# Kernel optimization log

Measured on AMD Instinct MI355X. Metric: run time of the kernel, lower is better.

Reference implementation:

```python
import jax, jax.numpy as jnp
import numpy as np

D_MODEL = 384
D_STATE = 64
D_CONV = 3
EXPAND = 2
HEADDIM = 64
NGROUPS = 1
CHUNK = 256
D_INNER = EXPAND * D_MODEL            # 768
NHEADS = D_INNER // HEADDIM           # 12
CONV_DIM = D_INNER + 2 * NGROUPS * D_STATE   # 896
D_IN_PROJ = 2 * D_INNER + 2 * NGROUPS * D_STATE + NHEADS  # 1676
EPS = 1e-5


def setup_inputs() -> dict:
    key = jax.random.key(0)
    ks = jax.random.split(key, 8)
    B, H, W = 16, 32, 32
    u = jax.random.normal(ks[0], (B, D_MODEL, H, W), jnp.float32)
    in_proj_w = jax.random.normal(ks[1], (D_IN_PROJ, D_MODEL), jnp.float32) / np.sqrt(D_MODEL)
    conv_w = jax.random.normal(ks[2], (CONV_DIM, 1, D_CONV, D_CONV), jnp.float32) / np.sqrt(D_CONV * D_CONV)
    conv_b = jax.random.normal(ks[3], (CONV_DIM,), jnp.float32) * 0.01
    # dt_bias init as in Mamba2.__init__
    dt = jnp.exp(jax.random.uniform(ks[4], (NHEADS,)) * (np.log(0.1) - np.log(0.001)) + np.log(0.001))
    dt = jnp.clip(dt, 1e-4, None)
    dt_bias = dt + jnp.log(-jnp.expm1(-dt))
    A_log = jnp.log(jax.random.uniform(ks[5], (NHEADS,), minval=1.0, maxval=16.0))
    D = jnp.ones((NHEADS,), jnp.float32)
    norm_w = jnp.ones((D_INNER,), jnp.float32)
    norm_b = jnp.zeros((D_INNER,), jnp.float32)
    out_proj_w = jax.random.normal(ks[6], (D_MODEL, D_INNER), jnp.float32) / np.sqrt(D_INNER)
    return {"u": u, "in_proj_w": in_proj_w, "conv_w": conv_w, "conv_b": conv_b,
            "dt_bias": dt_bias, "A_log": A_log, "D": D, "norm_w": norm_w,
            "norm_b": norm_b, "out_proj_w": out_proj_w}


def _chunk_scan(x, dt, A, Bm, Cm):
    """SSD chunked scan. x:(b,l,h,p) dt:(b,l,h) A:(h,) Bm,Cm:(b,l,g,n) -> (b,l,h,p)"""
    b, l, h, p = x.shape
    nc = l // CHUNK
    xc = x.reshape(b, nc, CHUNK, h, p)
    dtc = dt.reshape(b, nc, CHUNK, h)
    hpg = h // NGROUPS
    Bh = jnp.repeat(Bm.reshape(b, nc, CHUNK, NGROUPS, D_STATE), hpg, axis=3)  # (b,c,cs,h,n)
    Ch = jnp.repeat(Cm.reshape(b, nc, CHUNK, NGROUPS, D_STATE), hpg, axis=3)
    dA = dtc * A                                  # (b,c,cs,h)
    dA_cs = jnp.cumsum(dA, axis=2)                # cumulative log-decay within chunk
    # ---- intra-chunk (masked, attention-like) ----
    Lmat = jnp.exp(dA_cs[:, :, :, None, :] - dA_cs[:, :, None, :, :])  # (b,c,i,j,h)
    causal = jnp.tril(jnp.ones((CHUNK, CHUNK), bool))
    att = jnp.einsum('bcihn,bcjhn->bcijh', Ch, Bh) * Lmat * dtc[:, :, None, :, :]
    att = jnp.where(causal[None, None, :, :, None], att, 0.0)
    y_intra = jnp.einsum('bcijh,bcjhp->bcihp', att, xc)
    # ---- per-chunk end states ----
    decay_to_end = jnp.exp(dA_cs[:, :, -1:, :] - dA_cs)                 # (b,c,cs,h)
    states = jnp.einsum('bcjhn,bcjh,bcjhp->bchpn', Bh, decay_to_end * dtc, xc)
    chunk_decay = jnp.exp(dA_cs[:, :, -1, :])                           # (b,c,h)
    # ---- inter-chunk recurrence over the (few) chunks ----
    def step(carry, inp):
        st, dec = inp
        new = carry * dec[:, :, None, None] + st
        return new, carry  # emit state *before* this chunk
    init = jnp.zeros((b, h, p, D_STATE), x.dtype)
    _, prevs = jax.lax.scan(step, init, (jnp.moveaxis(states, 1, 0), jnp.moveaxis(chunk_decay, 1, 0)))
    prev_states = jnp.moveaxis(prevs, 0, 1)                             # (b,c,h,p,n)
    y_inter = jnp.einsum('bcihn,bcih,bchpn->bcihp', Ch, jnp.exp(dA_cs), prev_states)
    return (y_intra + y_inter).reshape(b, l, h, p)


def reference(u, in_proj_w, conv_w, conv_b, dt_bias, A_log, D, norm_w, norm_b, out_proj_w):
    B, C, H, W = u.shape
    L = H * W
    useq = u.reshape(B, C, L).transpose(0, 2, 1)                        # (B,L,C)
    zxbcdt = useq @ in_proj_w.T                                         # (B,L,D_IN_PROJ)
    z = zxbcdt[..., :D_INNER]
    xBC = zxbcdt[..., D_INNER:D_INNER + CONV_DIM]
    dt = jax.nn.softplus(zxbcdt[..., D_INNER + CONV_DIM:] + dt_bias)    # (B,L,NHEADS)
    # depthwise 3x3 conv over (H,W)
    xBC = xBC.reshape(B, H, W, CONV_DIM)
    kern = jnp.transpose(conv_w, (2, 3, 1, 0))                          # HWIO, groups=CONV_DIM
    xBC = jax.lax.conv_general_dilated(xBC, kern, (1, 1), 'SAME',
                                       dimension_numbers=('NHWC', 'HWIO', 'NHWC'),
                                       feature_group_count=CONV_DIM) + conv_b
    xBC = jax.nn.silu(xBC).reshape(B, L, CONV_DIM)
    x = xBC[..., :D_INNER].reshape(B, L, NHEADS, HEADDIM)
    Bm = xBC[..., D_INNER:D_INNER + NGROUPS * D_STATE].reshape(B, L, NGROUPS, D_STATE)
    Cm = xBC[..., D_INNER + NGROUPS * D_STATE:].reshape(B, L, NGROUPS, D_STATE)
    A = -jnp.exp(A_log)
    y = _chunk_scan(x, dt, A, Bm, Cm) + D[None, None, :, None] * x      # D skip per head
    y = y.reshape(B, L, D_INNER)
    # LayerNorm then gate by z (no activation on z, matching source)
    mu = jnp.mean(y, axis=-1, keepdims=True)
    var = jnp.var(y, axis=-1, keepdims=True)
    y = (y - mu) / jnp.sqrt(var + EPS) * norm_w + norm_b
    y = y * z
    out = y @ out_proj_w.T                                              # (B,L,C)
    return out.reshape(B, H, W, C).transpose(0, 3, 1, 2)
```

## Files before the change

kernel.cpp:

```cpp
#include <hip/hip_runtime.h>
#include <hip/hip_bf16.h>

#define B_    16
#define L_    1024
#define DM    384
#define DIP   1676
#define NIP   1664
#define DI    768
#define CONVD 896
#define NH    12
#define HD    64
#define DS    64
#define NCH   4
#define CH    256
#define EPS_  1e-5f

typedef unsigned short u16;
typedef unsigned int   u32;
typedef __attribute__((ext_vector_type(8))) _Float16 f16x8;
typedef __attribute__((ext_vector_type(4))) float f32x4;

union U4 { uint4 v; u16 s[8]; };

#define SWZ(row, slot) (((row) << 7) + ((((slot) ^ ((row) & 7)) & 7) << 4))

__device__ __forceinline__ u16 f2h(float v) { return __builtin_bit_cast(u16, (_Float16)v); }
__device__ __forceinline__ float h2f(u16 h) { return (float)__builtin_bit_cast(_Float16, h); }

__global__ __launch_bounds__(256) void k_prep(
    const float* __restrict__ u, const float* __restrict__ ipw,
    const float* __restrict__ opw,
    const float* __restrict__ dtb, const float* __restrict__ A_log,
    u16* __restrict__ Ah, u16* __restrict__ Whip, u16* __restrict__ Woh,
    float* __restrict__ dt, float* __restrict__ dAcs, float* __restrict__ cdecay)
{
  __shared__ float smem[32 * 129 + 8];
  const int bid = blockIdx.x;
  const int t = threadIdx.x;
  if (bid < 1536) {
    float (*Ls)[129] = (float(*)[129])smem;
    const int l0 = (bid & 7) * 128;
    const int k0 = ((bid >> 3) % 12) * 32;
    const int b  = bid / 96;
#pragma unroll
    for (int r = 0; r < 4; ++r) {
      int idx = r * 256 + t;
      int kk = idx >> 5, q = idx & 31;
      float4 v = *(const float4*)&u[((size_t)(b * DM + k0 + kk)) * L_ + l0 + q * 4];
      Ls[kk][q * 4 + 0] = v.x; Ls[kk][q * 4 + 1] = v.y;
      Ls[kk][q * 4 + 2] = v.z; Ls[kk][q * 4 + 3] = v.w;
    }
    __syncthreads();
#pragma unroll
    for (int it = 0; it < 2; ++it) {
      int task = it * 256 + t;
      int l = task >> 2, kq = (task & 3) * 8;
      u32 hw[4];
#pragma unroll
      for (int j = 0; j < 4; ++j) {
        u16 h0 = f2h(Ls[kq + 2 * j + 0][l]);
        u16 h1 = f2h(Ls[kq + 2 * j + 1][l]);
        hw[j] = (u32)h0 | ((u32)h1 << 16);
      }
      size_t off = ((size_t)(b * L_ + l0 + l)) * DM + k0 + kq;
      *(uint4*)&Ah[off] = make_uint4(hw[0], hw[1], hw[2], hw[3]);
    }
  } else if (bid < 2160) {
    int i = (bid - 1536) * 256 + t;
    if (i < NIP * DM / 4) {
      int e = i * 4;
      float4 v = *(const float4*)&ipw[e];
      u16 h[4] = {f2h(v.x), f2h(v.y), f2h(v.z), f2h(v.w)};
      *(uint2*)&Whip[e] = make_uint2((u32)h[0] | ((u32)h[1] << 16), (u32)h[2] | ((u32)h[3] << 16));
    }
  } else if (bid < 2448) {
    int i = (bid - 2160) * 256 + t;
    if (i < DM * DI / 4) {
      int e = i * 4;
      float4 v = *(const float4*)&opw[e];
      u16 h[4] = {f2h(v.x), f2h(v.y), f2h(v.z), f2h(v.w)};
      *(uint2*)&Woh[e] = make_uint2((u32)h[0] | ((u32)h[1] << 16), (u32)h[2] | ((u32)h[3] << 16));
    }
  } else {
    float* wdt = smem;
    float* ws4 = smem + DM;
    const int bb = bid - 2448;
    const int bc = bb & 63;
    const int h  = bb >> 6;
    const int b  = bc >> 2, l0 = (bc & 3) * 256;
    const int lane = t & 63, w = t >> 6;
    for (int i = t; i < DM; i += 256) wdt[i] = ipw[(size_t)(NIP + h) * DM + i];
    __syncthreads();
    const float* ub = u + (size_t)b * DM * L_ + l0 + t;
    float acc = 0.f;
#pragma unroll 8
    for (int k = 0; k < DM; ++k)
      acc = fmaf(ub[(size_t)k * L_], wdt[k], acc);
    const size_t row = (size_t)bc * 256 + t;
    float logit = acc + dtb[h];
    float dtv = (logit > 20.f) ? logit : log1pf(expf(logit));
    dt[row * NH + h] = dtv;
    float xv = dtv * (-expf(A_log[h]));
#pragma unroll
    for (int off = 1; off < 64; off <<= 1) {
      float y = __shfl_up(xv, off, 64);
      if (lane >= off) xv += y;
    }
    if (lane == 63) ws4[w] = xv;
    __syncthreads();
    float add = 0.f;
#pragma unroll
    for (int i = 0; i < 4; ++i) if (i < w) add += ws4[i];
    xv += add;
    dAcs[row * NH + h] = xv;
    if (t == 255) cdecay[bc * NH + h] = expf(xv);
  }
}

#define STAGE2S(bufbase, k0, KS) do {                                                           \
  _Pragma("unroll")                                                                             \
  for (int i_ = 0; i_ < 2; ++i_) {                                                              \
    int S_ = i_ * 256 + t;                                                                      \
    int m_ = S_ >> 2;                                                                           \
    int g_ = (S_ ^ (m_ >> 1)) & 3;                                                              \
    size_t goff_ = (size_t)m_ * (KS) + (k0) + g_ * 8;                                           \
    __builtin_amdgcn_global_load_lds((const __attribute__((address_space(1))) u32*)(g0 + goff_),\
        (__attribute__((address_space(3))) u32*)(lds + (bufbase) + S_ * 8), 16, 0, 0);          \
    __builtin_amdgcn_global_load_lds((const __attribute__((address_space(1))) u32*)(g2 + goff_),\
        (__attribute__((address_space(3))) u32*)(lds + (bufbase) + 4096 + S_ * 8), 16, 0, 0);   \
  }                                                                                             \
} while (0)

__global__ __launch_bounds__(256) void k_gemm1(
    const u16* __restrict__ Ah,
    const u16* __restrict__ Wh,
    u16* __restrict__ z, u16* __restrict__ xBC)
{
  __shared__ u16 lds[16384];
  const int t = threadIdx.x;
  const int lane = t & 63, wid = t >> 6;
  const int wr = wid >> 1, wc = wid & 1;
  const int gg = lane >> 4, mlo = lane & 15;
  const int xs = (blockIdx.x & 7) * 16 + (blockIdx.x >> 3);
  const int m0 = xs * 128, n0 = blockIdx.y * 128;
  f32x4 acc[4][4];
#pragma unroll
  for (int i = 0; i < 4; ++i)
#pragma unroll
    for (int j = 0; j < 4; ++j) acc[i][j] = (f32x4){0.f, 0.f, 0.f, 0.f};
  const u16* g0 = Ah + (size_t)m0 * DM;
  const u16* g2 = Wh + (size_t)n0 * DM;
  const int NT = DM / 32;
  STAGE2S(0, 0, DM);
  int cur = 0;
  for (int kt = 0; kt < NT; ++kt) {
    int ks = kt + 1; if (ks > NT - 1) ks = NT - 1;
    STAGE2S((cur ^ 1) * 8192, ks * 32, DM);
    asm volatile("s_waitcnt vmcnt(4)" ::: "memory");
    __builtin_amdgcn_s_barrier();
    const char* ldsb = (const char*)lds + cur * 16384;
    f16x8 fa[4], fb[4];
#pragma unroll
    for (int mf = 0; mf < 4; ++mf) {
      int m = wr * 64 + mf * 16 + mlo;
      int off = m * 64 + (((gg ^ (m >> 1)) & 3) << 4);
      fa[mf]  = *(const f16x8*)(ldsb + off);
    }
#pragma unroll
    for (int nf = 0; nf < 4; ++nf) {
      int n = wc * 64 + nf * 16 + mlo;
      int off = n * 64 + (((gg ^ (n >> 1)) & 3) << 4);
      fb[nf]  = *(const f16x8*)(ldsb + 8192 + off);
    }
#pragma unroll
    for (int mf = 0; mf < 4; ++mf)
#pragma unroll
      for (int nf = 0; nf < 4; ++nf)
        acc[mf][nf] = __builtin_amdgcn_mfma_f32_16x16x32_f16(fa[mf], fb[nf], acc[mf][nf], 0, 0, 0);
    __builtin_amdgcn_s_barrier();
    cur ^= 1;
  }
  const int rb = m0 + wr * 64 + (lane >> 4) * 4;
  const int cb = n0 + wc * 64 + mlo;
#pragma unroll
  for (int mf = 0; mf < 4; ++mf)
#pragma unroll
    for (int nf = 0; nf < 4; ++nf) {
      int col = cb + nf * 16;
#pragma unroll
      for (int r = 0; r < 4; ++r) {
        int row = rb + mf * 16 + r;
        float v = acc[mf][nf][r];
        if (col < DI) z[(size_t)row * DI + col] = f2h(v);
        else xBC[(size_t)row * CONVD + (col - DI)] = f2h(v);
      }
    }
}

__global__ __launch_bounds__(256) void k_gemm2(
    const u16* __restrict__ Ah,
    const u16* __restrict__ Bh,
    float* __restrict__ out)
{
  __shared__ u16 lds[16384];
  const int t = threadIdx.x;
  const int lane = t & 63, wid = t >> 6;
  const int wr = wid >> 1, wc = wid & 1;
  const int gg = lane >> 4, mlo = lane & 15;
  const int xs = (blockIdx.x & 7) * 16 + (blockIdx.x >> 3);
  const int m0 = xs * 128, n0 = blockIdx.y * 128;
  f32x4 acc[4][4];
#pragma unroll
  for (int i = 0; i < 4; ++i)
#pragma unroll
    for (int j = 0; j < 4; ++j) acc[i][j] = (f32x4){0.f, 0.f, 0.f, 0.f};
  const u16* g0 = Ah + (size_t)m0 * DI;
  const u16* g2 = Bh + (size_t)n0 * DI;
  const int NT = DI / 32;
  STAGE2S(0, 0, DI);
  int cur = 0;
  for (int kt = 0; kt < NT; ++kt) {
    int ks = kt + 1; if (ks > NT - 1) ks = NT - 1;
    STAGE2S((cur ^ 1) * 8192, ks * 32, DI);
    asm volatile("s_waitcnt vmcnt(4)" ::: "memory");
    __builtin_amdgcn_s_barrier();
    const char* ldsb = (const char*)lds + cur * 16384;
    f16x8 fa[4], fb[4];
#pragma unroll
    for (int mf = 0; mf < 4; ++mf) {
      int m = wr * 64 + mf * 16 + mlo;
      int off = m * 64 + (((gg ^ (m >> 1)) & 3) << 4);
      fa[mf]  = *(const f16x8*)(ldsb + off);
    }
#pragma unroll
    for (int nf = 0; nf < 4; ++nf) {
      int n = wc * 64 + nf * 16 + mlo;
      int off = n * 64 + (((gg ^ (n >> 1)) & 3) << 4);
      fb[nf]  = *(const f16x8*)(ldsb + 8192 + off);
    }
#pragma unroll
    for (int mf = 0; mf < 4; ++mf)
#pragma unroll
      for (int nf = 0; nf < 4; ++nf)
        acc[mf][nf] = __builtin_amdgcn_mfma_f32_16x16x32_f16(fa[mf], fb[nf], acc[mf][nf], 0, 0, 0);
    __builtin_amdgcn_s_barrier();
    cur ^= 1;
  }
  const int rb = m0 + wr * 64 + (lane >> 4) * 4;
  const int cb = n0 + wc * 64 + mlo;
#pragma unroll
  for (int mf = 0; mf < 4; ++mf)
#pragma unroll
    for (int nf = 0; nf < 4; ++nf) {
      int col = cb + nf * 16;
#pragma unroll
      for (int r = 0; r < 4; ++r) {
        int row = rb + mf * 16 + r;
        int b = row >> 10, l = row & 1023;
        out[((size_t)(b * DM + col)) * L_ + l] = acc[mf][nf][r];
      }
    }
}

#define CC 16
__global__ __launch_bounds__(256) void k_conv(
    const u16* __restrict__ xBC, const float* __restrict__ cw,
    const float* __restrict__ cb,
    u16* __restrict__ XTh,
    u16* __restrict__ Bh,
    u16* __restrict__ Chh)
{
  __shared__ float Ls[18][32][CC];
  const int t  = threadIdx.x;
  const int c0 = blockIdx.x * CC;
  const int h0 = blockIdx.y * 16;
  const int b  = blockIdx.z;
#pragma unroll
  for (int k = 0; k < 9; ++k) {
    int f = k * 256 + t;
    int fc4 = f & 3, fw = (f >> 2) & 31, fr = f >> 7;
    int h = h0 + fr - 1;
    U4 v; v.v = make_uint4(0, 0, 0, 0);
    if (h >= 0 && h < 32) {
      uint2 p = *(const uint2*)&xBC[((size_t)(b * 1024 + h * 32 + fw)) * CONVD + c0 + fc4 * 4];
      v.v.x = p.x; v.v.y = p.y;
    }
    Ls[fr][fw][fc4 * 4 + 0] = h2f(v.s[0]);
    Ls[fr][fw][fc4 * 4 + 1] = h2f(v.s[1]);
    Ls[fr][fw][fc4 * 4 + 2] = h2f(v.s[2]);
    Ls[fr][fw][fc4 * 4 + 3] = h2f(v.s[3]);
  }
  const int c4 = t & 3;
  const int w  = (t >> 2) & 31;
  const int hb = t >> 7;
  float wt[4][9];
  float bias[4];
#pragma unroll
  for (int j = 0; j < 4; ++j) {
    int c = c0 + c4 * 4 + j;
    bias[j] = cb[c];
#pragma unroll
    for (int kb = 0; kb < 9; ++kb) wt[j][kb] = cw[c * 9 + kb];
  }
  __syncthreads();
  const bool isx = (c0 < DI);
  u16 xh16[8][4];
#pragma unroll
  for (int k = 0; k < 8; ++k) {
    int h = hb * 8 + k;
    float acc[4] = {bias[0], bias[1], bias[2], bias[3]};
#pragma unroll
    for (int dh = 0; dh < 3; ++dh) {
#pragma unroll
      for (int dw = -1; dw <= 1; ++dw) {
        int ww = w + dw;
        if (ww < 0 || ww > 31) continue;
        const float* p = &Ls[h + dh][ww][c4 * 4];
        int kb = dh * 3 + (dw + 1);
#pragma unroll
        for (int j = 0; j < 4; ++j) acc[j] = fmaf(p[j], wt[j][kb], acc[j]);
      }
    }
    float s4[4];
#pragma unroll
    for (int j = 0; j < 4; ++j) { float v = acc[j]; s4[j] = v / (1.f + expf(-v)); }
    if (isx) {
#pragma unroll
      for (int j = 0; j < 4; ++j) xh16[k][j] = f2h(s4[j]);
    } else {
      size_t row = (size_t)b * 1024 + (h0 + h) * 32 + w;
      u16 hv[4] = {f2h(s4[0]), f2h(s4[1]), f2h(s4[2]), f2h(s4[3])};
      uint2 hp = make_uint2((u32)hv[0] | ((u32)hv[1] << 16), (u32)hv[2] | ((u32)hv[3] << 16));
      int c = c0 + c4 * 4;
      if (c < DI + DS) *(uint2*)&Bh[row * DS + (c - DI)] = hp;
      else             *(uint2*)&Chh[row * DS + (c - DI - DS)] = hp;
    }
  }
  if (isx) {
    __syncthreads();
    u16* Ls2 = (u16*)Ls;
#pragma unroll
    for (int k = 0; k < 8; ++k) {
      int pos = (hb * 8 + k) * 32 + w;
#pragma unroll
      for (int j = 0; j < 4; ++j)
        Ls2[(c4 * 4 + j) * 512 + pos] = xh16[k][j];
    }
    __syncthreads();
    const int hh = c0 >> 6;
    const int pb = c0 & 63;
#pragma unroll
    for (int i = 0; i < 4; ++i) {
      int cid = i * 256 + t;
      int pl = cid >> 6, rem = cid & 63;
      int jbl = rem >> 3, slot = rem & 7;
      int labs = h0 * 32 + jbl * 64;
      size_t tile = ((size_t)(b * 4 + (labs >> 8)) * NH + hh) * 4 + ((labs >> 6) & 3);
      *(uint4*)((char*)XTh + tile * 8192 + SWZ(pb + pl, slot)) =
          *(const uint4*)&Ls2[pl * 512 + jbl * 64 + slot * 8];
    }
  }
}

#define STAGE_XT(tileByte) do {                                                                   \
  _Pragma("unroll")                                                                               \
  for (int i_ = 0; i_ < 2; ++i_) {                                                                \
    int S_ = i_ * 256 + t;                                                                        \
    __builtin_amdgcn_global_load_lds(                                                             \
        (const __attribute__((address_space(1))) u32*)((const char*)XTh + (tileByte) + S_ * 16),  \
        (__attribute__((address_space(3))) u32*)((char*)Xh_t + S_ * 16), 16, 0, 0);               \
  }                                                                                               \
} while (0)

__global__ __launch_bounds__(256) void k_states(
    const u16* __restrict__ XTh,
    const u16* __restrict__ Bh,
    const float* __restrict__ dt, const float* __restrict__ dAcs,
    float* __restrict__ states)
{
  __shared__ u16 bpackB[64 * 65];
  __shared__ u16 BTh_t[4096];
  __shared__ u16 Xh_t[4096];
  __shared__ float wall[256];
  const int bc = blockIdx.x;
  const int hh = blockIdx.y;
  const int t  = threadIdx.x;
  const int lane = t & 63, w = t >> 6;
  const int mlo = lane & 15, gg = lane >> 4;
  const int r = t >> 2, q = (t & 3) * 16;
  const size_t base = (size_t)bc * 256;
  const float last = dAcs[(base + 255) * NH + hh];
  wall[t] = __expf(last - dAcs[(base + t) * NH + hh]) * dt[(base + t) * NH + hh];
  f32x4 acc[4];
#pragma unroll
  for (int i = 0; i < 4; ++i) acc[i] = (f32x4){0.f, 0.f, 0.f, 0.f};
  for (int jt = 0; jt < 4; ++jt) {
    const int j0 = jt * 64;
    __syncthreads();
    STAGE_XT(((size_t)(bc * NH + hh) * 4 + jt) * 8192);
    {
      const u16* bhp = &Bh[(size_t)(base + j0 + r) * DS + q];
      U4 H0, H1;
      H0.v = *(const uint4*)bhp; H1.v = *(const uint4*)(bhp + 8);
#pragma unroll
      for (int k = 0; k < 8; ++k) {
        bpackB[r * 65 + q + k]     = H0.s[k];
        bpackB[r * 65 + q + 8 + k] = H1.s[k];
      }
    }
    __syncthreads();
#pragma unroll
    for (int c = 0; c < 2; ++c) {
      U4 BH;
#pragma unroll
      for (int jj = 0; jj < 8; ++jj) {
        int j = q + c * 8 + jj;
        BH.s[jj] = f2h(h2f(bpackB[j * 65 + r]) * wall[j0 + j]);
      }
      *(uint4*)((char*)BTh_t + SWZ(r, (q >> 3) + c)) = BH.v;
    }
    __syncthreads();
#pragma unroll
    for (int s = 0; s < 2; ++s) {
      f16x8 fah = *(const f16x8*)((const char*)Xh_t + SWZ(w * 16 + mlo, s * 4 + gg));
#pragma unroll
      for (int nf = 0; nf < 4; ++nf) {
        f16x8 fbh = *(const f16x8*)((const char*)BTh_t + SWZ(nf * 16 + mlo, s * 4 + gg));
        acc[nf] = __builtin_amdgcn_mfma_f32_16x16x32_f16(fah, fbh, acc[nf], 0, 0, 0);
      }
    }
  }
  const size_t sb = ((size_t)(bc * NH + hh)) << 12;
#pragma unroll
  for (int nf = 0; nf < 4; ++nf)
#pragma unroll
    for (int reg = 0; reg < 4; ++reg) {
      int p = w * 16 + (lane >> 4) * 4 + reg;
      int n = nf * 16 + mlo;
      states[sb + (size_t)p * 64 + n] = acc[nf][reg];
    }
}

__global__ __launch_bounds__(256) void k_scanc(
    const float* __restrict__ states, const float* __restrict__ cdecay,
    float* __restrict__ prev)
{
  int tid = blockIdx.x * 256 + threadIdx.x;
  int pn  = tid & 4095;
  int rem = tid >> 12;
  int hh  = rem % NH;
  int b   = rem / NH;
  float carry = 0.f;
#pragma unroll
  for (int c = 0; c < 4; ++c) {
    size_t idx = ((size_t)((b * 4 + c) * NH + hh) << 12) + pn;
    prev[idx] = carry;
    carry = carry * cdecay[(b * 4 + c) * NH + hh] + states[idx];
  }
}

__global__ __launch_bounds__(256) void k_y(
    const u16* __restrict__ XTh,
    const u16* __restrict__ Chg, const u16* __restrict__ Bhg,
    const float* __restrict__ dtp, const float* __restrict__ dAcs,
    const float* __restrict__ prev, const float* __restrict__ Dp,
    u16* __restrict__ y)
{
  __shared__ u16 Pb_t[4096];
  __shared__ u16 Xh_t[4096];
  __shared__ u16 att_t[4096];
  __shared__ float dAc_s[256], dt_s[256], ei_s[128];
  const int bc = blockIdx.x;
  const int hh = blockIdx.y;
  const int z  = blockIdx.z;
  const int it0 = z * 2;
  const int t  = threadIdx.x;
  const int lane = t & 63, w = t >> 6;
  const int mlo = lane & 15, gg = lane >> 4;
  const int r = t >> 2, q = (t & 3) * 16;
  const int slot0 = q >> 3;
  const size_t base = (size_t)bc * 256;
  {
    float da = dAcs[(base + t) * NH + hh];
    dAc_s[t] = da;
    dt_s[t]  = dtp[(base + t) * NH + hh];
    if (t < 128) ei_s[t] = __expf(dAcs[(base + z * 128 + t) * NH + hh]);
  }
  {
    const float* pp = &prev[(((size_t)(bc * NH + hh)) << 12) + (size_t)r * 64 + q];
    U4 H0, H1;
#pragma unroll
    for (int k = 0; k < 16; ++k) {
      u16 h = f2h(pp[k]);
      if (k < 8) H0.s[k] = h; else H1.s[k - 8] = h;
    }
    *(uint4*)((char*)Pb_t + SWZ(r, slot0))     = H0.v;
    *(uint4*)((char*)Pb_t + SWZ(r, slot0 + 1)) = H1.v;
  }
  __syncthreads();
  f16x8 fc[2][2];
#pragma unroll
  for (int iti = 0; iti < 2; ++iti)
#pragma unroll
    for (int s = 0; s < 2; ++s)
      fc[iti][s] = *(const f16x8*)&Chg[(size_t)(base + (it0 + iti) * 64 + w * 16 + mlo) * DS +
                                       (s * 4 + gg) * 8];
  f32x4 accy[2][4];
#pragma unroll
  for (int i = 0; i < 2; ++i)
#pragma unroll
    for (int j = 0; j < 4; ++j) accy[i][j] = (f32x4){0.f, 0.f, 0.f, 0.f};
#pragma unroll
  for (int s = 0; s < 2; ++s)
#pragma unroll
    for (int pf = 0; pf < 4; ++pf) {
      f16x8 fph = *(const f16x8*)((const char*)Pb_t + SWZ(pf * 16 + mlo, s * 4 + gg));
#pragma unroll
      for (int iti = 0; iti < 2; ++iti)
        accy[iti][pf] = __builtin_amdgcn_mfma_f32_16x16x32_f16(fc[iti][s], fph, accy[iti][pf], 0, 0, 0);
    }
  const int ilb = w * 16 + (lane >> 4) * 4;
#pragma unroll
  for (int iti = 0; iti < 2; ++iti)
#pragma unroll
    for (int pf = 0; pf < 4; ++pf)
#pragma unroll
      for (int reg = 0; reg < 4; ++reg)
        accy[iti][pf][reg] *= ei_s[iti * 64 + ilb + reg];

  u32 xdv[2][8];
  for (int jt = 0; jt <= it0 + 1; ++jt) {
    __syncthreads();
    STAGE_XT(((size_t)(bc * NH + hh) * 4 + jt) * 8192);
    {
      const u16* bh = &Bhg[(size_t)(base + jt * 64 + r) * DS + q];
      U4 V0, V1;
      V0.v = *(const uint4*)bh; V1.v = *(const uint4*)(bh + 8);
      float wj = dt_s[jt * 64 + r];
#pragma unroll
      for (int k = 0; k < 8; ++k) {
        V0.s[k] = f2h(h2f(V0.s[k]) * wj);
        V1.s[k] = f2h(h2f(V1.s[k]) * wj);
      }
      *(uint4*)((char*)Pb_t + SWZ(r, slot0))     = V0.v;
      *(uint4*)((char*)Pb_t + SWZ(r, slot0 + 1)) = V1.v;
    }
    __syncthreads();
#pragma unroll
    for (int iti = 0; iti < 2; ++iti) {
      if (jt == it0 + iti) {
#pragma unroll
        for (int pf = 0; pf < 4; ++pf)
#pragma unroll
          for (int rp = 0; rp < 2; ++rp) {
            int j0l = ilb + rp * 2;
            u16 a = *(const u16*)((const char*)Xh_t + SWZ(pf * 16 + mlo, j0l >> 3) + (j0l & 7) * 2);
            u16 b2 = *(const u16*)((const char*)Xh_t + SWZ(pf * 16 + mlo, (j0l + 1) >> 3) + ((j0l + 1) & 7) * 2);
            xdv[iti][pf * 2 + rp] = (u32)a | ((u32)b2 << 16);
          }
      }
    }
#pragma unroll
    for (int iti = 0; iti < 2; ++iti) {
      const int ita = it0 + iti;
      if (jt > ita) continue;
      f32x4 g[4];
#pragma unroll
      for (int i = 0; i < 4; ++i) g[i] = (f32x4){0.f, 0.f, 0.f, 0.f};
#pragma unroll
      for (int s = 0; s < 2; ++s)
#pragma unroll
        for (int jf = 0; jf < 4; ++jf) {
          f16x8 fbh = *(const f16x8*)((const char*)Pb_t + SWZ(jf * 16 + mlo, s * 4 + gg));
          g[jf] = __builtin_amdgcn_mfma_f32_16x16x32_f16(fc[iti][s], fbh, g[jf], 0, 0, 0);
        }
#pragma unroll
      for (int jf = 0; jf < 4; ++jf)
#pragma unroll
        for (int reg = 0; reg < 4; ++reg) {
          int il = ita * 64 + ilb + reg;
          int jl = jt * 64 + jf * 16 + mlo;
          float av = (jl <= il) ? g[jf][reg] * __expf(dAc_s[il] - dAc_s[jl]) : 0.f;
          *(u16*)((char*)att_t + SWZ(il & 63, (jl & 63) >> 3) + (jl & 7) * 2) = f2h(av);
        }
#pragma unroll
      for (int s = 0; s < 2; ++s) {
        f16x8 fa = *(const f16x8*)((const char*)att_t + SWZ(w * 16 + mlo, s * 4 + gg));
#pragma unroll
        for (int pf = 0; pf < 4; ++pf) {
          f16x8 fxh = *(const f16x8*)((const char*)Xh_t + SWZ(pf * 16 + mlo, s * 4 + gg));
          accy[iti][pf] = __builtin_amdgcn_mfma_f32_16x16x32_f16(fa, fxh, accy[iti][pf], 0, 0, 0);
        }
      }
    }
  }
  const float Dh = Dp[hh];
#pragma unroll
  for (int iti = 0; iti < 2; ++iti)
#pragma unroll
    for (int pf = 0; pf < 4; ++pf)
#pragma unroll
      for (int reg = 0; reg < 4; ++reg) {
        size_t row = base + (it0 + iti) * 64 + ilb + reg;
        int col = hh * HD + pf * 16 + mlo;
        u32 pk = xdv[iti][pf * 2 + (reg >> 1)];
        u16 xv = (reg & 1) ? (u16)(pk >> 16) : (u16)pk;
        y[row * DI + col] = f2h(accy[iti][pf][reg] + Dh * h2f(xv));
      }
}

__global__ __launch_bounds__(256) void k_norm(
    const u16* __restrict__ z, const float* __restrict__ nw,
    const float* __restrict__ nb, const u16* __restrict__ y,
    u16* __restrict__ yh)
{
  __shared__ float rs[4], rq[4];
  const size_t row = blockIdx.x;
  const int t = threadIdx.x;
  float v[3];
  float s = 0.f, sq = 0.f;
#pragma unroll
  for (int r = 0; r < 3; ++r) {
    v[r] = h2f(y[row * DI + r * 256 + t]);
    s += v[r];
    sq = fmaf(v[r], v[r], sq);
  }
#pragma unroll
  for (int off = 32; off > 0; off >>= 1) {
    s  += __shfl_down(s, off, 64);
    sq += __shfl_down(sq, off, 64);
  }
  const int wid = t >> 6, lane = t & 63;
  if (lane == 0) { rs[wid] = s; rq[wid] = sq; }
  __syncthreads();
  if (t == 0) {
    rs[0] = rs[0] + rs[1] + rs[2] + rs[3];
    rq[0] = rq[0] + rq[1] + rq[2] + rq[3];
  }
  __syncthreads();
  const float mu   = rs[0] * (1.f / DI);
  const float var  = rq[0] * (1.f / DI) - mu * mu;
  const float rstd = 1.f / sqrtf(var + EPS_);
#pragma unroll
  for (int r = 0; r < 3; ++r) {
    int d = r * 256 + t;
    float o = (v[r] - mu) * rstd * nw[d] + nb[d];
    float p = o * h2f(z[row * DI + d]);
    yh[row * DI + d] = f2h(p);
  }
}

extern "C" void kernel_launch(void* const* d_in, const int* in_sizes, int n_in,
                              void* d_out, int out_size, void* d_ws, size_t ws_size,
                              hipStream_t stream)
{
  const float* u    = (const float*)d_in[0];
  const float* ipw  = (const float*)d_in[1];
  const float* cw   = (const float*)d_in[2];
  const float* cb   = (const float*)d_in[3];
  const float* dtb  = (const float*)d_in[4];
  const float* Alog = (const float*)d_in[5];
  const float* Dp   = (const float*)d_in[6];
  const float* nw   = (const float*)d_in[7];
  const float* nb   = (const float*)d_in[8];
  const float* opw  = (const float*)d_in[9];
  float* out = (float*)d_out;

  float* ws = (float*)d_ws;
  size_t off = 0;
  u16*   z16     = (u16*)(ws + off); off += (size_t)B_ * L_ * DI / 2;
  u16*   xBC16   = (u16*)(ws + off); off += (size_t)B_ * L_ * CONVD / 2;
  float* dt_buf  = ws + off; off += (size_t)B_ * L_ * NH;
  float* x_buf   = ws + off; off += (size_t)B_ * L_ * DI;
  u16*   y16     = (u16*)(ws + off); off += (size_t)B_ * L_ * DI / 2;
  u16*   Bh_buf  = (u16*)(ws + off); off += (size_t)B_ * L_ * DS / 2;
  u16*   Ch_buf  = (u16*)(ws + off); off += (size_t)B_ * L_ * DS / 2;
  float* dAcs    = ws + off; off += (size_t)B_ * L_ * NH;
  float* cdec    = ws + off; off += (size_t)B_ * NCH * NH;
  float* st_buf  = ws + off; off += (size_t)B_ * NCH * NH * HD * DS;
  float* pv_buf  = ws + off; off += (size_t)B_ * NCH * NH * HD * DS;
  u16*   Woh     = (u16*)(ws + off); off += (size_t)DM * DI / 2;
  u16*   XTh_buf = (u16*)(ws + off); off += (size_t)B_ * NCH * NH * 4 * 4096 / 2;

  u16* Ah = (u16*)x_buf;
  u16* Whip = Ah + (size_t)B_ * L_ * DM;
  u16* yh = (u16*)x_buf;

  hipLaunchKernelGGL(k_prep, dim3(3216), dim3(256), 0, stream,
                     u, ipw, opw, dtb, Alog, Ah, Whip, Woh, dt_buf, dAcs, cdec);
  hipLaunchKernelGGL(k_gemm1, dim3(128, 13), dim3(256), 0, stream,
                     Ah, Whip, z16, xBC16);
  hipLaunchKernelGGL(k_conv, dim3(56, 2, 16), dim3(256), 0, stream,
                     xBC16, cw, cb, XTh_buf, Bh_buf, Ch_buf);
  hipLaunchKernelGGL(k_states, dim3(64, 12), dim3(256), 0, stream,
                     XTh_buf, Bh_buf, dt_buf, dAcs, st_buf);
  hipLaunchKernelGGL(k_scanc, dim3(3072), dim3(256), 0, stream, st_buf, cdec, pv_buf);
  hipLaunchKernelGGL(k_y, dim3(64, 12, 2), dim3(256), 0, stream,
                     XTh_buf, Ch_buf, Bh_buf, dt_buf, dAcs, pv_buf, Dp, y16);
  hipLaunchKernelGGL(k_norm, dim3(16384), dim3(256), 0, stream, z16, nw, nb, y16, yh);
  hipLaunchKernelGGL(k_gemm2, dim3(128, 3), dim3(256), 0, stream, yh, Woh, out);
}
```

Before: 191.3 us.

## Fuse LayerNorm+gate into out-proj GEMM and inter-chunk scan into k_y

Removes the separate k_norm kernel by computing per-row mean/rstd inside the output GEMM and applying normalization and z gating while staging the A tile into LDS. Removes k_scanc by having k_y recompute the carried state from fp16 chunk states and decays, and k_states now writes fp16 states. This cuts two launches and the fp32 states/prev and normalized-y round trips through global memory. In exchange, y and z are now loaded synchronously per k-step without a double buffer, and row statistics are recomputed in each of the three N-tile blocks.

```diff
diff --git a/kernel.cpp b/kernel.cpp
--- a/kernel.cpp
+++ b/kernel.cpp
@@ -197,53 +197,123 @@
     }
 }
 
-__global__ __launch_bounds__(256) void k_gemm2(
-    const u16* __restrict__ Ah,
-    const u16* __restrict__ Bh,
+__global__ __launch_bounds__(256) void k_gemm2n(
+    const u16* __restrict__ y16, const u16* __restrict__ z16,
+    const float* __restrict__ nw, const float* __restrict__ nb,
+    const u16* __restrict__ Woh,
     float* __restrict__ out)
 {
-  __shared__ u16 lds[16384];
+  __shared__ u16 Ab[4096];
+  __shared__ u16 Wb[8192];
+  __shared__ float wln[DI], bln[DI];
+  __shared__ float muL[128], rsL[128];
   const int t = threadIdx.x;
   const int lane = t & 63, wid = t >> 6;
   const int wr = wid >> 1, wc = wid & 1;
   const int gg = lane >> 4, mlo = lane & 15;
   const int xs = (blockIdx.x & 7) * 16 + (blockIdx.x >> 3);
   const int m0 = xs * 128, n0 = blockIdx.y * 128;
+  for (int i = t; i < DI; i += 256) { wln[i] = nw[i]; bln[i] = nb[i]; }
+  {
+    const int row = t >> 1, half = t & 1;
+    const u16* yp = y16 + (size_t)(m0 + row) * DI + half * 384;
+    float s = 0.f, sq = 0.f;
+    for (int i = 0; i < 48; ++i) {
+      U4 v; v.v = *(const uint4*)(yp + i * 8);
+#pragma unroll
+      for (int k = 0; k < 8; ++k) { float f = h2f(v.s[k]); s += f; sq = fmaf(f, f, sq); }
+    }
+    s  += __shfl_xor(s, 1, 64);
+    sq += __shfl_xor(sq, 1, 64);
+    if (half == 0) {
+      float mu = s * (1.f / DI);
+      float var = sq * (1.f / DI) - mu * mu;
+      muL[row] = mu;
+      rsL[row] = 1.f / sqrtf(var + EPS_);
+    }
+  }
   f32x4 acc[4][4];
 #pragma unroll
   for (int i = 0; i < 4; ++i)
 #pragma unroll
     for (int j = 0; j < 4; ++j) acc[i][j] = (f32x4){0.f, 0.f, 0.f, 0.f};
-  const u16* g0 = Ah + (size_t)m0 * DI;
-  const u16* g2 = Bh + (size_t)n0 * DI;
+  const u16* g2 = Woh + (size_t)n0 * DI;
   const int NT = DI / 32;
-  STAGE2S(0, 0, DI);
+  __syncthreads();
+#pragma unroll
+  for (int i_ = 0; i_ < 2; ++i_) {
+    int S_ = i_ * 256 + t;
+    int n_ = S_ >> 2;
+    int g_ = (S_ ^ (n_ >> 1)) & 3;
+    size_t goff_ = (size_t)n_ * DI + g_ * 8;
+    __builtin_amdgcn_global_load_lds((const __attribute__((address_space(1))) u32*)(g2 + goff_),
+        (__attribute__((address_space(3))) u32*)(Wb + S_ * 8), 16, 0, 0);
+  }
   int cur = 0;
   for (int kt = 0; kt < NT; ++kt) {
-    int ks = kt + 1; if (ks > NT - 1) ks = NT - 1;
-    STAGE2S((cur ^ 1) * 8192, ks * 32, DI);
-    asm volatile("s_waitcnt vmcnt(4)" ::: "memory");
     __builtin_amdgcn_s_barrier();
-    const char* ldsb = (const char*)lds + cur * 16384;
+    const int k0 = kt * 32;
+    U4 yv[2], zv[2];
+#pragma unroll
+    for (int i_ = 0; i_ < 2; ++i_) {
+      int S_ = i_ * 256 + t;
+      int m_ = S_ >> 2;
+      int g_ = (S_ ^ (m_ >> 1)) & 3;
+      size_t go = (size_t)(m0 + m_) * DI + k0 + g_ * 8;
+      yv[i_].v = *(const uint4*)(y16 + go);
+      zv[i_].v = *(const uint4*)(z16 + go);
+    }
+    if (kt + 1 < NT) {
+#pragma unroll
+      for (int i_ = 0; i_ < 2; ++i_) {
+        int S_ = i_ * 256 + t;
+        int n_ = S_ >> 2;
+        int g_ = (S_ ^ (n_ >> 1)) & 3;
+        size_t goff_ = (size_t)n_ * DI + (kt + 1) * 32 + g_ * 8;
+        __builtin_amdgcn_global_load_lds((const __attribute__((address_space(1))) u32*)(g2 + goff_),
+            (__attribute__((address_space(3))) u32*)(Wb + (cur ^ 1) * 4096 + S_ * 8), 16, 0, 0);
+      }
+    }
+#pragma unroll
+    for (int i_ = 0; i_ < 2; ++i_) {
+      int S_ = i_ * 256 + t;
+      int m_ = S_ >> 2;
+      int g_ = (S_ ^ (m_ >> 1)) & 3;
+      float mu = muL[m_], a = rsL[m_];
+      float nma = mu * a;
+      U4 o;
+#pragma unroll
+      for (int j = 0; j < 8; ++j) {
+        int d = k0 + g_ * 8 + j;
+        float v = h2f(yv[i_].s[j]);
+        float on = fmaf(fmaf(v, a, -nma), wln[d], bln[d]);
+        o.s[j] = f2h(on * h2f(zv[i_].s[j]));
+      }
+      *(uint4*)((char*)Ab + S_ * 16) = o.v;
+    }
+    asm volatile("s_waitcnt lgkmcnt(0)" ::: "memory");
+    asm volatile("s_waitcnt vmcnt(2)" ::: "memory");
+    __builtin_amdgcn_s_barrier();
+    const char* ldA = (const char*)Ab;
+    const char* ldW = (const char*)Wb + cur * 8192;
     f16x8 fa[4], fb[4];
 #pragma unroll
     for (int mf = 0; mf < 4; ++mf) {
       int m = wr * 64 + mf * 16 + mlo;
       int off = m * 64 + (((gg ^ (m >> 1)) & 3) << 4);
-      fa[mf]  = *(const f16x8*)(ldsb + off);
+      fa[mf] = *(const f16x8*)(ldA + off);
     }
 #pragma unroll
     for (int nf = 0; nf < 4; ++nf) {
       int n = wc * 64 + nf * 16 + mlo;
       int off = n * 64 + (((gg ^ (n >> 1)) & 3) << 4);
-      fb[nf]  = *(const f16x8*)(ldsb + 8192 + off);
+      fb[nf] = *(const f16x8*)(ldW + off);
     }
 #pragma unroll
     for (int mf = 0; mf < 4; ++mf)
 #pragma unroll
       for (int nf = 0; nf < 4; ++nf)
         acc[mf][nf] = __builtin_amdgcn_mfma_f32_16x16x32_f16(fa[mf], fb[nf], acc[mf][nf], 0, 0, 0);
-    __builtin_amdgcn_s_barrier();
     cur ^= 1;
   }
   const int rb = m0 + wr * 64 + (lane >> 4) * 4;
@@ -376,7 +446,7 @@
     const u16* __restrict__ XTh,
     const u16* __restrict__ Bh,
     const float* __restrict__ dt, const float* __restrict__ dAcs,
-    float* __restrict__ states)
+    u16* __restrict__ st16)
 {
   __shared__ u16 bpackB[64 * 65];
   __shared__ u16 BTh_t[4096];
@@ -437,33 +507,16 @@
     for (int reg = 0; reg < 4; ++reg) {
       int p = w * 16 + (lane >> 4) * 4 + reg;
       int n = nf * 16 + mlo;
-      states[sb + (size_t)p * 64 + n] = acc[nf][reg];
-    }
-}
-
-__global__ __launch_bounds__(256) void k_scanc(
-    const float* __restrict__ states, const float* __restrict__ cdecay,
-    float* __restrict__ prev)
-{
-  int tid = blockIdx.x * 256 + threadIdx.x;
-  int pn  = tid & 4095;
-  int rem = tid >> 12;
-  int hh  = rem % NH;
-  int b   = rem / NH;
-  float carry = 0.f;
-#pragma unroll
-  for (int c = 0; c < 4; ++c) {
-    size_t idx = ((size_t)((b * 4 + c) * NH + hh) << 12) + pn;
-    prev[idx] = carry;
-    carry = carry * cdecay[(b * 4 + c) * NH + hh] + states[idx];
-  }
+      st16[sb + (size_t)p * 64 + n] = f2h(acc[nf][reg]);
+    }
 }
 
 __global__ __launch_bounds__(256) void k_y(
     const u16* __restrict__ XTh,
     const u16* __restrict__ Chg, const u16* __restrict__ Bhg,
     const float* __restrict__ dtp, const float* __restrict__ dAcs,
-    const float* __restrict__ prev, const float* __restrict__ Dp,
+    const u16* __restrict__ st16, const float* __restrict__ cdec,
+    const float* __restrict__ Dp,
     u16* __restrict__ y)
 {
   __shared__ u16 Pb_t[4096];
@@ -487,13 +540,24 @@
     if (t < 128) ei_s[t] = __expf(dAcs[(base + z * 128 + t) * NH + hh]);
   }
   {
-    const float* pp = &prev[(((size_t)(bc * NH + hh)) << 12) + (size_t)r * 64 + q];
+    const int b = bc >> 2, cchunk = bc & 3;
+    float carry[16];
+#pragma unroll
+    for (int k = 0; k < 16; ++k) carry[k] = 0.f;
+    for (int c2 = 0; c2 < cchunk; ++c2) {
+      float dec = cdec[(b * 4 + c2) * NH + hh];
+      const u16* sp = &st16[(((size_t)((b * 4 + c2) * NH + hh)) << 12) + (size_t)r * 64 + q];
+      U4 S0, S1;
+      S0.v = *(const uint4*)sp; S1.v = *(const uint4*)(sp + 8);
+#pragma unroll
+      for (int k = 0; k < 8; ++k) {
+        carry[k]     = carry[k]     * dec + h2f(S0.s[k]);
+        carry[k + 8] = carry[k + 8] * dec + h2f(S1.s[k]);
+      }
+    }
     U4 H0, H1;
 #pragma unroll
-    for (int k = 0; k < 16; ++k) {
-      u16 h = f2h(pp[k]);
-      if (k < 8) H0.s[k] = h; else H1.s[k - 8] = h;
-    }
+    for (int k = 0; k < 8; ++k) { H0.s[k] = f2h(carry[k]); H1.s[k] = f2h(carry[k + 8]); }
     *(uint4*)((char*)Pb_t + SWZ(r, slot0))     = H0.v;
     *(uint4*)((char*)Pb_t + SWZ(r, slot0 + 1)) = H1.v;
   }
@@ -607,47 +671,6 @@
         u16 xv = (reg & 1) ? (u16)(pk >> 16) : (u16)pk;
         y[row * DI + col] = f2h(accy[iti][pf][reg] + Dh * h2f(xv));
       }
-}
-
-__global__ __launch_bounds__(256) void k_norm(
-    const u16* __restrict__ z, const float* __restrict__ nw,
-    const float* __restrict__ nb, const u16* __restrict__ y,
-    u16* __restrict__ yh)
-{
-  __shared__ float rs[4], rq[4];
-  const size_t row = blockIdx.x;
-  const int t = threadIdx.x;
-  float v[3];
-  float s = 0.f, sq = 0.f;
-#pragma unroll
-  for (int r = 0; r < 3; ++r) {
-    v[r] = h2f(y[row * DI + r * 256 + t]);
-    s += v[r];
-    sq = fmaf(v[r], v[r], sq);
-  }
-#pragma unroll
-  for (int off = 32; off > 0; off >>= 1) {
-    s  += __shfl_down(s, off, 64);
-    sq += __shfl_down(sq, off, 64);
-  }
-  const int wid = t >> 6, lane = t & 63;
-  if (lane == 0) { rs[wid] = s; rq[wid] = sq; }
-  __syncthreads();
-  if (t == 0) {
-    rs[0] = rs[0] + rs[1] + rs[2] + rs[3];
-    rq[0] = rq[0] + rq[1] + rq[2] + rq[3];
-  }
-  __syncthreads();
-  const float mu   = rs[0] * (1.f / DI);
-  const float var  = rq[0] * (1.f / DI) - mu * mu;
-  const float rstd = 1.f / sqrtf(var + EPS_);
-#pragma unroll
-  for (int r = 0; r < 3; ++r) {
-    int d = r * 256 + t;
-    float o = (v[r] - mu) * rstd * nw[d] + nb[d];
-    float p = o * h2f(z[row * DI + d]);
-    yh[row * DI + d] = f2h(p);
-  }
 }
 
 extern "C" void kernel_launch(void* const* d_in, const int* in_sizes, int n_in,
@@ -677,14 +700,12 @@
   u16*   Ch_buf  = (u16*)(ws + off); off += (size_t)B_ * L_ * DS / 2;
   float* dAcs    = ws + off; off += (size_t)B_ * L_ * NH;
   float* cdec    = ws + off; off += (size_t)B_ * NCH * NH;
-  float* st_buf  = ws + off; off += (size_t)B_ * NCH * NH * HD * DS;
-  float* pv_buf  = ws + off; off += (size_t)B_ * NCH * NH * HD * DS;
+  u16*   st16    = (u16*)(ws + off); off += (size_t)B_ * NCH * NH * HD * DS / 2;
   u16*   Woh     = (u16*)(ws + off); off += (size_t)DM * DI / 2;
   u16*   XTh_buf = (u16*)(ws + off); off += (size_t)B_ * NCH * NH * 4 * 4096 / 2;
 
   u16* Ah = (u16*)x_buf;
   u16* Whip = Ah + (size_t)B_ * L_ * DM;
-  u16* yh = (u16*)x_buf;
 
   hipLaunchKernelGGL(k_prep, dim3(3216), dim3(256), 0, stream,
                      u, ipw, opw, dtb, Alog, Ah, Whip, Woh, dt_buf, dAcs, cdec);
@@ -693,10 +714,9 @@
   hipLaunchKernelGGL(k_conv, dim3(56, 2, 16), dim3(256), 0, stream,
                      xBC16, cw, cb, XTh_buf, Bh_buf, Ch_buf);
   hipLaunchKernelGGL(k_states, dim3(64, 12), dim3(256), 0, stream,
-                     XTh_buf, Bh_buf, dt_buf, dAcs, st_buf);
-  hipLaunchKernelGGL(k_scanc, dim3(3072), dim3(256), 0, stream, st_buf, cdec, pv_buf);
+                     XTh_buf, Bh_buf, dt_buf, dAcs, st16);
   hipLaunchKernelGGL(k_y, dim3(64, 12, 2), dim3(256), 0, stream,
-                     XTh_buf, Ch_buf, Bh_buf, dt_buf, dAcs, pv_buf, Dp, y16);
-  hipLaunchKernelGGL(k_norm, dim3(16384), dim3(256), 0, stream, z16, nw, nb, y16, yh);
-  hipLaunchKernelGGL(k_gemm2, dim3(128, 3), dim3(256), 0, stream, yh, Woh, out);
+                     XTh_buf, Ch_buf, Bh_buf, dt_buf, dAcs, st16, cdec, Dp, y16);
+  hipLaunchKernelGGL(k_gemm2n, dim3(128, 3), dim3(256), 0, stream,
+                     y16, z16, nw, nb, Woh, out);
 }
```

New measurement: 193.0 us. About the same (+0.9%).

## Fuse inter-chunk state scan into k_y and store chunk states as fp16

Applied to the files above, without the earlier changes.

Removes the separate k_scanc kernel and folds the inter-chunk carry recurrence into k_y. Each k_y block now recomputes its incoming state from the fp16 per-chunk states of the earlier chunks. k_states writes its states in fp16 instead of fp32, which halves the state traffic and drops the prev buffer's write and read. In exchange the carry work is repeated across both z blocks and the earlier chunks, and states are rounded to fp16 before accumulation, which adds some precision loss.

```diff
diff --git a/kernel.cpp b/kernel.cpp
--- a/kernel.cpp
+++ b/kernel.cpp
@@ -376,7 +376,7 @@
     const u16* __restrict__ XTh,
     const u16* __restrict__ Bh,
     const float* __restrict__ dt, const float* __restrict__ dAcs,
-    float* __restrict__ states)
+    u16* __restrict__ st16)
 {
   __shared__ u16 bpackB[64 * 65];
   __shared__ u16 BTh_t[4096];
@@ -437,33 +437,16 @@
     for (int reg = 0; reg < 4; ++reg) {
       int p = w * 16 + (lane >> 4) * 4 + reg;
       int n = nf * 16 + mlo;
-      states[sb + (size_t)p * 64 + n] = acc[nf][reg];
-    }
-}
-
-__global__ __launch_bounds__(256) void k_scanc(
-    const float* __restrict__ states, const float* __restrict__ cdecay,
-    float* __restrict__ prev)
-{
-  int tid = blockIdx.x * 256 + threadIdx.x;
-  int pn  = tid & 4095;
-  int rem = tid >> 12;
-  int hh  = rem % NH;
-  int b   = rem / NH;
-  float carry = 0.f;
-#pragma unroll
-  for (int c = 0; c < 4; ++c) {
-    size_t idx = ((size_t)((b * 4 + c) * NH + hh) << 12) + pn;
-    prev[idx] = carry;
-    carry = carry * cdecay[(b * 4 + c) * NH + hh] + states[idx];
-  }
+      st16[sb + (size_t)p * 64 + n] = f2h(acc[nf][reg]);
+    }
 }
 
 __global__ __launch_bounds__(256) void k_y(
     const u16* __restrict__ XTh,
     const u16* __restrict__ Chg, const u16* __restrict__ Bhg,
     const float* __restrict__ dtp, const float* __restrict__ dAcs,
-    const float* __restrict__ prev, const float* __restrict__ Dp,
+    const u16* __restrict__ st16, const float* __restrict__ cdec,
+    const float* __restrict__ Dp,
     u16* __restrict__ y)
 {
   __shared__ u16 Pb_t[4096];
@@ -487,13 +470,24 @@
     if (t < 128) ei_s[t] = __expf(dAcs[(base + z * 128 + t) * NH + hh]);
   }
   {
-    const float* pp = &prev[(((size_t)(bc * NH + hh)) << 12) + (size_t)r * 64 + q];
+    const int b = bc >> 2, cchunk = bc & 3;
+    float carry[16];
+#pragma unroll
+    for (int k = 0; k < 16; ++k) carry[k] = 0.f;
+    for (int c2 = 0; c2 < cchunk; ++c2) {
+      float dec = cdec[(b * 4 + c2) * NH + hh];
+      const u16* sp = &st16[(((size_t)((b * 4 + c2) * NH + hh)) << 12) + (size_t)r * 64 + q];
+      U4 S0, S1;
+      S0.v = *(const uint4*)sp; S1.v = *(const uint4*)(sp + 8);
+#pragma unroll
+      for (int k = 0; k < 8; ++k) {
+        carry[k]     = carry[k]     * dec + h2f(S0.s[k]);
+        carry[k + 8] = carry[k + 8] * dec + h2f(S1.s[k]);
+      }
+    }
     U4 H0, H1;
 #pragma unroll
-    for (int k = 0; k < 16; ++k) {
-      u16 h = f2h(pp[k]);
-      if (k < 8) H0.s[k] = h; else H1.s[k - 8] = h;
-    }
+    for (int k = 0; k < 8; ++k) { H0.s[k] = f2h(carry[k]); H1.s[k] = f2h(carry[k + 8]); }
     *(uint4*)((char*)Pb_t + SWZ(r, slot0))     = H0.v;
     *(uint4*)((char*)Pb_t + SWZ(r, slot0 + 1)) = H1.v;
   }
@@ -677,8 +671,7 @@
   u16*   Ch_buf  = (u16*)(ws + off); off += (size_t)B_ * L_ * DS / 2;
   float* dAcs    = ws + off; off += (size_t)B_ * L_ * NH;
   float* cdec    = ws + off; off += (size_t)B_ * NCH * NH;
-  float* st_buf  = ws + off; off += (size_t)B_ * NCH * NH * HD * DS;
-  float* pv_buf  = ws + off; off += (size_t)B_ * NCH * NH * HD * DS;
+  u16*   st16    = (u16*)(ws + off); off += (size_t)B_ * NCH * NH * HD * DS / 2;
   u16*   Woh     = (u16*)(ws + off); off += (size_t)DM * DI / 2;
   u16*   XTh_buf = (u16*)(ws + off); off += (size_t)B_ * NCH * NH * 4 * 4096 / 2;
 
@@ -693,10 +686,9 @@
   hipLaunchKernelGGL(k_conv, dim3(56, 2, 16), dim3(256), 0, stream,
                      xBC16, cw, cb, XTh_buf, Bh_buf, Ch_buf);
   hipLaunchKernelGGL(k_states, dim3(64, 12), dim3(256), 0, stream,
-                     XTh_buf, Bh_buf, dt_buf, dAcs, st_buf);
-  hipLaunchKernelGGL(k_scanc, dim3(3072), dim3(256), 0, stream, st_buf, cdec, pv_buf);
+                     XTh_buf, Bh_buf, dt_buf, dAcs, st16);
   hipLaunchKernelGGL(k_y, dim3(64, 12, 2), dim3(256), 0, stream,
-                     XTh_buf, Ch_buf, Bh_buf, dt_buf, dAcs, pv_buf, Dp, y16);
+                     XTh_buf, Ch_buf, Bh_buf, dt_buf, dAcs, st16, cdec, Dp, y16);
   hipLaunchKernelGGL(k_norm, dim3(16384), dim3(256), 0, stream, z16, nw, nb, y16, yh);
   hipLaunchKernelGGL(k_gemm2, dim3(128, 3), dim3(256), 0, stream, yh, Woh, out);
 }
```

After: 187.5 us. 2.0% less time.
